# Performance work log

Hardware: AMD Instinct MI355X
Metric: run time of the kernel (lower is better)

Reference implementation:

```python
import jax, jax.numpy as jnp
import numpy as np

IN_FEATURES = 4096
OUT_FEATURES = 4096
WBITS = 4
GROUPSIZE = 128
PACK_FACTOR = 32 // WBITS  # 8
MASK = (1 << WBITS) - 1    # 15


def setup_inputs() -> dict:
    key = jax.random.key(0)
    k1, k2, k3, k4, k5 = jax.random.split(key, 5)
    x = jax.random.normal(k1, (4, 2048, IN_FEATURES), dtype=jnp.float32)
    # Packed 4-bit weights: (in_features*wbits//32, out_features) int32 words.
    qweight = jax.random.randint(k2, (IN_FEATURES * WBITS // 32, OUT_FEATURES),
                                 jnp.iinfo(jnp.int32).min, jnp.iinfo(jnp.int32).max,
                                 dtype=jnp.int32)
    num_groups = IN_FEATURES // GROUPSIZE  # 32
    # Packed zero points: (num_groups, out_features*wbits//32) int32 words.
    qzeros = jax.random.randint(k3, (num_groups, OUT_FEATURES * WBITS // 32),
                                jnp.iinfo(jnp.int32).min, jnp.iinfo(jnp.int32).max,
                                dtype=jnp.int32)
    scales = jax.random.uniform(k4, (num_groups, OUT_FEATURES), dtype=jnp.float32,
                                minval=0.001, maxval=0.02)
    bias = jax.random.normal(k5, (OUT_FEATURES,), dtype=jnp.float32)
    return {"x": x, "qweight": qweight, "qzeros": qzeros, "scales": scales, "bias": bias}


def _unpack4(packed, axis_len):
    """Unpack int32 words along a new inner axis of PACK_FACTOR 4-bit nibbles.

    packed: (..., n_words) -> (..., n_words*PACK_FACTOR) int32 in [0, 15].
    """
    shifts = (jnp.arange(PACK_FACTOR, dtype=jnp.int32) * WBITS)
    nib = (packed[..., :, None] >> shifts) & MASK  # (..., n_words, PACK_FACTOR)
    return nib.reshape(*packed.shape[:-1], axis_len)


def reference(x, qweight, qzeros, scales, bias):
    # Unpack weights: qweight is packed along in_features (dim 0).
    # (in/8, 8, out) -> (in, out) int nibbles.
    shifts = (jnp.arange(PACK_FACTOR, dtype=jnp.int32) * WBITS)
    wq = ((qweight[:, None, :] >> shifts[None, :, None]) & MASK)
    wq = wq.reshape(IN_FEATURES, OUT_FEATURES)  # [in, out] int32 in [0,15]
    # Unpack zeros: packed along out_features (dim 1); AutoGPTQ stores zero-1,
    # so add 1 back at dequant time.
    zq = _unpack4(qzeros, OUT_FEATURES) + 1  # [num_groups, out]
    g_idx = jnp.arange(IN_FEATURES, dtype=jnp.int32) // GROUPSIZE  # [in]
    # Per-group affine dequant: W[i,o] = s[g(i),o] * (wq[i,o] - z[g(i),o])
    W = scales[g_idx] * (wq - zq[g_idx]).astype(scales.dtype)  # [in, out]
    # y = x @ W + b  (x: [b, s, in])
    return jnp.einsum('bsi,io->bso', x, W) + bias
```

## Files before the change

kernel.cpp:

```cpp
#include <hip/hip_runtime.h>
#include <hip/hip_bf16.h>
#include <stdint.h>


#define M_TOT 8192
#define N_TOT 4096
#define K_TOT 4096
#define NT    (K_TOT / 64)

using bf16x8 = __attribute__((ext_vector_type(8))) __bf16;
using f32x4  = __attribute__((ext_vector_type(4))) float;

__device__ __forceinline__ unsigned short f2bf(float f) {
  unsigned u = __builtin_bit_cast(unsigned, f);
  u += 0x7fffu + ((u >> 16) & 1u);
  return (unsigned short)(u >> 16);
}

__global__ void cvt_x_kernel(const float* __restrict__ x,
                             unsigned short* __restrict__ xb, int n) {
  int stride = gridDim.x * blockDim.x * 8;
  for (int i = (blockIdx.x * blockDim.x + threadIdx.x) * 8; i < n; i += stride) {
    float4 a = *reinterpret_cast<const float4*>(x + i);
    float4 b = *reinterpret_cast<const float4*>(x + i + 4);
    unsigned short o[8] = {f2bf(a.x), f2bf(a.y), f2bf(a.z), f2bf(a.w),
                           f2bf(b.x), f2bf(b.y), f2bf(b.z), f2bf(b.w)};
    *reinterpret_cast<uint4*>(xb + i) = *reinterpret_cast<const uint4*>(o);
  }
}

__global__ void dequant_wt_kernel(const int* __restrict__ qweight,
                                  const int* __restrict__ qzeros,
                                  const float* __restrict__ scales,
                                  unsigned short* __restrict__ wt) {
  int t = blockIdx.x * blockDim.x + threadIdx.x;
  int nn = t >> 9;
  int kw = t & 511;
  int g  = kw >> 4;
  unsigned w = (unsigned)qweight[kw * N_TOT + nn];
  float s = scales[g * N_TOT + nn];
  unsigned zw = (unsigned)qzeros[g * (N_TOT / 8) + (nn >> 3)];
  float z = (float)(((zw >> ((nn & 7) * 4)) & 15u) + 1u);
  unsigned short o[8];
#pragma unroll
  for (int j = 0; j < 8; ++j) {
    float v = s * ((float)((w >> (4 * j)) & 15u) - z);
    o[j] = f2bf(v);
  }
  *reinterpret_cast<uint4*>(wt + (size_t)nn * K_TOT + kw * 8) =
      *reinterpret_cast<const uint4*>(o);
}

__device__ __forceinline__ void gll16(const unsigned short* g, const unsigned short* l) {
  __builtin_amdgcn_global_load_lds(
      (const __attribute__((address_space(1))) void*)(uintptr_t)g,
      (__attribute__((address_space(3))) void*)(uintptr_t)l, 16, 0, 0);
}

__global__ __launch_bounds__(512, 2) void gemm_8phase_kernel(
    const unsigned short* __restrict__ A,
    const unsigned short* __restrict__ B,
    const float* __restrict__ bias,
    float* __restrict__ C) {
  __shared__ __align__(16) unsigned short As[2 * 256 * 64];
  __shared__ __align__(16) unsigned short Bs[2 * 256 * 64];

  int bid = blockIdx.x;
  int swz = (bid & 7) * 64 + (bid >> 3);
  int bm = swz & 31, bn = swz >> 5;
  int m0 = bm * 256, n0 = bn * 256;

  int t = threadIdx.x;
  int lane = t & 63;
  int wave = t >> 6;
  int wr = wave >> 2, wc = wave & 3;
  int lr = lane & 15, kq = lane >> 4;

  int rowL0 = t >> 3;
  int jlog  = ((t & 7) ^ (rowL0 & 7)) * 8;
  const unsigned short* aG = A + (size_t)(m0 + rowL0) * K_TOT + jlog;
  const unsigned short* bG = B + (size_t)(n0 + rowL0) * K_TOT + jlog;

  unsigned rbA = (unsigned)((wr * 128 + lr) * 128 + ((kq * 16) ^ ((lr & 7) << 4)));
  unsigned rbB = (unsigned)((wc * 64  + lr) * 128 + ((kq * 16) ^ ((lr & 7) << 4)));

  f32x4 acc[8][4] = {};
  bf16x8 av[2][2][2];
  bf16x8 bh[2][4][2];

#define STAGE(matG, ldsArr, tile, h)                                              \
  do {                                                                            \
    const unsigned short* _g = (matG) + (size_t)(h) * 128 * K_TOT +               \
                               (size_t)(tile) * 64;                               \
    const unsigned short* _l = (ldsArr) + ((tile) & 1) * 16384 + (h) * 8192 +     \
                               t * 8;                                             \
    gll16(_g, _l);                                                                \
    gll16(_g + (size_t)64 * K_TOT, _l + 4096);                                    \
  } while (0)

  STAGE(aG, As, 0, 0);
  STAGE(aG, As, 0, 1);
  STAGE(bG, Bs, 0, 0);
  STAGE(bG, Bs, 0, 1);
  STAGE(bG, Bs, 1, 0);
  STAGE(bG, Bs, 1, 1);
  asm volatile("s_waitcnt vmcnt(4)" ::: "memory");
  __builtin_amdgcn_s_barrier();
  __builtin_amdgcn_sched_barrier(0);

  {
    const char* aB0 = (const char*)As;
    const char* bB0 = (const char*)Bs;
#pragma unroll
    for (int n = 0; n < 4; ++n)
#pragma unroll
      for (int s = 0; s < 2; ++s)
        bh[0][n][s] = *(const bf16x8*)(bB0 + ((rbB + n * 2048) ^ (s * 64)));
#pragma unroll
    for (int mm = 0; mm < 2; ++mm)
#pragma unroll
      for (int s = 0; s < 2; ++s)
        av[0][mm][s] = *(const bf16x8*)(aB0 + ((rbA + mm * 2048) ^ (s * 64)));
  }

#pragma unroll 2
  for (int tt = 0; tt < NT; ++tt) {
    const char* aBuf = (const char*)As + (tt & 1) * 32768;

#pragma unroll
    for (int q = 0; q < 4; ++q) {
      if (q < 3) {
#pragma unroll
        for (int mm = 0; mm < 2; ++mm)
#pragma unroll
          for (int s = 0; s < 2; ++s)
            av[(q + 1) & 1][mm][s] = *(const bf16x8*)(
                aBuf + ((rbA + (2 * (q + 1) + mm) * 2048) ^ (s * 64)));
      } else if (tt + 1 < NT) {
        const char* aN = (const char*)As + ((tt + 1) & 1) * 32768;
        const char* bN = (const char*)Bs + ((tt + 1) & 1) * 32768;
#pragma unroll
        for (int n = 0; n < 4; ++n)
#pragma unroll
          for (int s = 0; s < 2; ++s)
            bh[(tt + 1) & 1][n][s] = *(const bf16x8*)(bN + ((rbB + n * 2048) ^ (s * 64)));
#pragma unroll
        for (int mm = 0; mm < 2; ++mm)
#pragma unroll
          for (int s = 0; s < 2; ++s)
            av[0][mm][s] = *(const bf16x8*)(aN + ((rbA + mm * 2048) ^ (s * 64)));
      }
      __builtin_amdgcn_sched_barrier(0);

      __builtin_amdgcn_s_setprio(1);
#pragma unroll
      for (int s = 0; s < 2; ++s)
#pragma unroll
        for (int mm = 0; mm < 2; ++mm)
#pragma unroll
          for (int n = 0; n < 4; ++n)
            acc[2 * q + mm][n] = __builtin_amdgcn_mfma_f32_16x16x32_bf16(
                av[q & 1][mm][s], bh[tt & 1][n][s], acc[2 * q + mm][n], 0, 0, 0);
      __builtin_amdgcn_s_setprio(0);

      if (q == 0 && tt + 1 < NT) STAGE(aG, As, tt + 1, 0);
      if (q == 1 && tt + 1 < NT) STAGE(aG, As, tt + 1, 1);
      if (q == 2) {
        if (tt + 2 < NT) STAGE(bG, Bs, tt + 2, 0);
        if (tt >= NT - 3) asm volatile("s_waitcnt vmcnt(0)" ::: "memory");
        else              asm volatile("s_waitcnt vmcnt(2)" ::: "memory");
      }
      if (q == 3 && tt + 2 < NT) STAGE(bG, Bs, tt + 2, 1);
      __builtin_amdgcn_s_barrier();
    }
  }
#undef STAGE

#pragma unroll
  for (int n = 0; n < 4; ++n) {
    int ncol = n0 + wc * 64 + n * 16 + lr;
    float bz = bias[ncol];
#pragma unroll
    for (int m = 0; m < 8; ++m) {
      int mrow = m0 + wr * 128 + m * 16 + kq * 4;
#pragma unroll
      for (int r = 0; r < 4; ++r)
        C[(size_t)(mrow + r) * N_TOT + ncol] = acc[m][n][r] + bz;
    }
  }
}

extern "C" void kernel_launch(void* const* d_in, const int* in_sizes, int n_in,
                              void* d_out, int out_size, void* d_ws, size_t ws_size,
                              hipStream_t stream) {
  const float* x       = (const float*)d_in[0];
  const int*   qweight = (const int*)d_in[1];
  const int*   qzeros  = (const int*)d_in[2];
  const float* scales  = (const float*)d_in[3];
  const float* bias    = (const float*)d_in[4];
  float* out = (float*)d_out;

  const size_t xb_bytes = (size_t)M_TOT * K_TOT * 2;
  const size_t wt_bytes = (size_t)N_TOT * K_TOT * 2;
  if (ws_size < xb_bytes + wt_bytes) return;

  unsigned short* Xb = (unsigned short*)d_ws;
  unsigned short* Wt = (unsigned short*)((char*)d_ws + xb_bytes);

  cvt_x_kernel<<<2048, 256, 0, stream>>>(x, Xb, M_TOT * K_TOT);
  dequant_wt_kernel<<<(N_TOT * 512) / 256, 256, 0, stream>>>(qweight, qzeros, scales, Wt);

  dim3 grid((M_TOT / 256) * (N_TOT / 256));
  gemm_8phase_kernel<<<grid, 512, 0, stream>>>(Xb, Wt, bias, out);
}
```

Baseline: 289.8 us.

## Triple-buffer A tile in LDS to prefetch two K-tiles ahead

```diff
diff --git a/kernel.cpp b/kernel.cpp
--- a/kernel.cpp
+++ b/kernel.cpp
@@ -62,7 +62,7 @@
     const unsigned short* __restrict__ B,
     const float* __restrict__ bias,
     float* __restrict__ C) {
-  __shared__ __align__(16) unsigned short As[2 * 256 * 64];
+  __shared__ __align__(16) unsigned short As[3 * 256 * 64];
   __shared__ __align__(16) unsigned short Bs[2 * 256 * 64];
 
   int bid = blockIdx.x;
@@ -88,23 +88,24 @@
   bf16x8 av[2][2][2];
   bf16x8 bh[2][4][2];
 
-#define STAGE(matG, ldsArr, tile, h)                                              \
+#define STAGE(matG, ldsBase, tile, h)                                             \
   do {                                                                            \
     const unsigned short* _g = (matG) + (size_t)(h) * 128 * K_TOT +               \
                                (size_t)(tile) * 64;                               \
-    const unsigned short* _l = (ldsArr) + ((tile) & 1) * 16384 + (h) * 8192 +     \
-                               t * 8;                                             \
+    const unsigned short* _l = (ldsBase) + (h) * 8192 + t * 8;                    \
     gll16(_g, _l);                                                                \
     gll16(_g + (size_t)64 * K_TOT, _l + 4096);                                    \
   } while (0)
 
-  STAGE(aG, As, 0, 0);
-  STAGE(aG, As, 0, 1);
-  STAGE(bG, Bs, 0, 0);
-  STAGE(bG, Bs, 0, 1);
-  STAGE(bG, Bs, 1, 0);
-  STAGE(bG, Bs, 1, 1);
-  asm volatile("s_waitcnt vmcnt(4)" ::: "memory");
+  STAGE(aG, As,         0, 0);
+  STAGE(aG, As,         0, 1);
+  STAGE(bG, Bs,         0, 0);
+  STAGE(bG, Bs,         0, 1);
+  STAGE(aG, As + 16384, 1, 0);
+  STAGE(aG, As + 16384, 1, 1);
+  STAGE(bG, Bs + 16384, 1, 0);
+  STAGE(bG, Bs + 16384, 1, 1);
+  asm volatile("s_waitcnt vmcnt(8)" ::: "memory");
   __builtin_amdgcn_s_barrier();
   __builtin_amdgcn_sched_barrier(0);
 
@@ -125,7 +126,9 @@
 
 #pragma unroll 2
   for (int tt = 0; tt < NT; ++tt) {
-    const char* aBuf = (const char*)As + (tt & 1) * 32768;
+    const char* aBuf = (const char*)As + (tt % 3) * 32768;
+    unsigned short* aStage = As + ((tt + 2) % 3) * 16384;
+    unsigned short* bStage = Bs + (tt & 1) * 16384;
 
 #pragma unroll
     for (int q = 0; q < 4; ++q) {
@@ -136,19 +139,26 @@
           for (int s = 0; s < 2; ++s)
             av[(q + 1) & 1][mm][s] = *(const bf16x8*)(
                 aBuf + ((rbA + (2 * (q + 1) + mm) * 2048) ^ (s * 64)));
-      } else if (tt + 1 < NT) {
-        const char* aN = (const char*)As + ((tt + 1) & 1) * 32768;
-        const char* bN = (const char*)Bs + ((tt + 1) & 1) * 32768;
-#pragma unroll
-        for (int n = 0; n < 4; ++n)
-#pragma unroll
-          for (int s = 0; s < 2; ++s)
-            bh[(tt + 1) & 1][n][s] = *(const bf16x8*)(bN + ((rbB + n * 2048) ^ (s * 64)));
-#pragma unroll
-        for (int mm = 0; mm < 2; ++mm)
-#pragma unroll
-          for (int s = 0; s < 2; ++s)
-            av[0][mm][s] = *(const bf16x8*)(aN + ((rbA + mm * 2048) ^ (s * 64)));
+      } else {
+        if (tt >= NT - 2) asm volatile("s_waitcnt vmcnt(0)" ::: "memory");
+        else              asm volatile("s_waitcnt vmcnt(6)" ::: "memory");
+        __builtin_amdgcn_s_barrier();
+        __builtin_amdgcn_sched_barrier(0);
+        if (tt + 1 < NT) {
+          const char* aN = (const char*)As + ((tt + 1) % 3) * 32768;
+          const char* bN = (const char*)Bs + ((tt + 1) & 1) * 32768;
+#pragma unroll
+          for (int n = 0; n < 4; ++n)
+#pragma unroll
+            for (int s = 0; s < 2; ++s)
+              bh[(tt + 1) & 1][n][s] =
+                  *(const bf16x8*)(bN + ((rbB + n * 2048) ^ (s * 64)));
+#pragma unroll
+          for (int mm = 0; mm < 2; ++mm)
+#pragma unroll
+            for (int s = 0; s < 2; ++s)
+              av[0][mm][s] = *(const bf16x8*)(aN + ((rbA + mm * 2048) ^ (s * 64)));
+        }
       }
       __builtin_amdgcn_sched_barrier(0);
 
@@ -163,14 +173,12 @@
                 av[q & 1][mm][s], bh[tt & 1][n][s], acc[2 * q + mm][n], 0, 0, 0);
       __builtin_amdgcn_s_setprio(0);
 
-      if (q == 0 && tt + 1 < NT) STAGE(aG, As, tt + 1, 0);
-      if (q == 1 && tt + 1 < NT) STAGE(aG, As, tt + 1, 1);
-      if (q == 2) {
-        if (tt + 2 < NT) STAGE(bG, Bs, tt + 2, 0);
-        if (tt >= NT - 3) asm volatile("s_waitcnt vmcnt(0)" ::: "memory");
-        else              asm volatile("s_waitcnt vmcnt(2)" ::: "memory");
+      if (tt + 2 < NT) {
+        if (q == 0) STAGE(aG, aStage, tt + 2, 0);
+        if (q == 1) STAGE(aG, aStage, tt + 2, 1);
+        if (q == 2) STAGE(bG, bStage, tt + 2, 0);
+        if (q == 3) STAGE(bG, bStage, tt + 2, 1);
       }
-      if (q == 3 && tt + 2 < NT) STAGE(bG, Bs, tt + 2, 1);
       __builtin_amdgcn_s_barrier();
     }
   }
```

New measurement: 354.2 us. +22.2%, slower.
